# Optimization experiments

Hardware: AMD Instinct MI355X
Metric: run time of the kernel (lower is better)

Reference implementation:

```python
import jax, jax.numpy as jnp
import numpy as np

U, I, D, E = 8192, 8192, 64, 1048576  # users, items, emb dim, nnz of adjacency


def spmm(row, col, val, x, n):
    """Sparse (COO) @ dense: y[r] += val * x[c], like torch.sparse.mm."""
    return jax.ops.segment_sum(val[:, None] * x[col], row, num_segments=n)


def setup_inputs() -> dict:
    key = jax.random.key(0)
    k1, k2, k3, k4, k5, k6 = jax.random.split(key, 6)
    users_emb = jax.random.normal(k1, (U, D), dtype=jnp.float32) * 0.1  # nn.init.normal_(std=0.1)
    items_emb = jax.random.normal(k2, (I, D), dtype=jnp.float32) * 0.1
    edge_row = jax.random.randint(k3, (E,), 0, U + I, dtype=jnp.int32)
    edge_col = jax.random.randint(k4, (E,), 0, U + I, dtype=jnp.int32)
    # positive normalized adjacency values (stand-in for D^-1/2 A D^-1/2 entries)
    edge_val = jax.random.uniform(k5, (E,), dtype=jnp.float32) / 64.0
    # sparse 0/1 interaction matrix densified, as in labels = interaction_mat.toarray()
    labels = (jax.random.uniform(k6, (U, I)) < 0.02).astype(jnp.float32)
    return {"users_emb": users_emb, "items_emb": items_emb,
            "edge_row": edge_row, "edge_col": edge_col,
            "edge_val": edge_val, "labels": labels, "n_layers": 3}


def reference(users_emb, items_emb, edge_row, edge_col, edge_val, labels, n_layers):
    n = users_emb.shape[0] + items_emb.shape[0]
    u = users_emb.shape[0]
    all_emb = jnp.concatenate([users_emb, items_emb], axis=0)  # [n, D]
    # stack + mean over (n_layers+1) layer outputs == online accumulation
    acc = all_emb
    for _ in range(n_layers):
        all_emb = spmm(edge_row, edge_col, edge_val, all_emb, n)
        acc = acc + all_emb
    light_out = acc / jnp.float32(n_layers + 1)
    user_emb = light_out[:u]   # [U, D]
    item_emb = light_out[u:]   # [I, D]
    scores = user_emb @ item_emb.T  # [U, I]
    # BCEWithLogitsLoss (mean reduction): logaddexp(0, s) - s*y
    loss = jnp.mean(jnp.logaddexp(jnp.float32(0.0), scores) - scores * labels)
    return (loss, user_emb, item_emb)
```

## Files before the change

### kernel.cpp

```cpp
#include <hip/hip_runtime.h>

#define U_N 8192
#define N_N 16384
#define E_N 1048576
#define CAP 128
#define CSTRIDE 16

typedef __attribute__((ext_vector_type(8)))  short short8;
typedef __attribute__((ext_vector_type(16))) float f32x16;


__device__ __forceinline__ float bfu(ushort u) {
    union { unsigned v; float f; } c; c.v = (unsigned)u << 16; return c.f;
}
__device__ __forceinline__ ushort f2bf(float f) {
    union { float f; unsigned u; } c; c.f = f;
    return (ushort)((c.u + 0x7fffu + ((c.u >> 16) & 1u)) >> 16);
}

__global__ void k_prep(const float* __restrict__ ue, const float* __restrict__ ie,
                       ushort* __restrict__ xb, float* __restrict__ acc,
                       unsigned* __restrict__ cnt) {
    int i = blockIdx.x * blockDim.x + threadIdx.x;
    const int HU = U_N * 64 / 4;
    float4 v = (i < HU) ? ((const float4*)ue)[i] : ((const float4*)ie)[i - HU];
    ((float4*)acc)[i] = v;
    ushort4 b;
    b.x = f2bf(v.x); b.y = f2bf(v.y); b.z = f2bf(v.z); b.w = f2bf(v.w);
    ((ushort4*)xb)[i] = b;
    if (i < 65536) ((uint4*)cnt)[i] = make_uint4(0, 0, 0, 0);
}

__global__ __launch_bounds__(256) void k_mask(const float* __restrict__ labels,
                                              unsigned* __restrict__ mask) {
    int tid = blockIdx.x * 256 + threadIdx.x;
    const int stride = 2048 * 256;
    #pragma unroll 4
    for (int it = 0; it < 32; ++it) {
        int g = tid + it * stride;
        float4 v = ((const float4*)labels)[g];
        unsigned nib = (v.x != 0.f ? 1u : 0u) | (v.y != 0.f ? 2u : 0u)
                     | (v.z != 0.f ? 4u : 0u) | (v.w != 0.f ? 8u : 0u);
        unsigned wv = nib << ((g & 7) * 4);
        wv |= __shfl_xor(wv, 1);
        wv |= __shfl_xor(wv, 2);
        wv |= __shfl_xor(wv, 4);
        if ((threadIdx.x & 7) == 0) mask[g >> 3] = wv;
    }
}

__global__ void k_bucket(const int* __restrict__ row, const int* __restrict__ col,
                         const float* __restrict__ val, unsigned* __restrict__ cnt,
                         unsigned* __restrict__ buckets) {
    int e = blockIdx.x * blockDim.x + threadIdx.x;
    if (e < E_N) {
        int r = row[e];
        unsigned p = atomicAdd(&cnt[r * CSTRIDE], 1u);
        if (p < CAP)
            buckets[(size_t)r * CAP + p] = (unsigned)col[e] | ((unsigned)f2bf(val[e]) << 16);
    }
}

#define REC_FMA(rec)                                                       \
    {   unsigned _rc = (rec);                                              \
        float _xv = bfu(x[(_rc & 0xFFFFu) * 64 + lane]);                   \
        a = fmaf(bfu((ushort)(_rc >> 16)), _xv, a); }

__global__ void k_spmm(const unsigned* __restrict__ cnt, const unsigned* __restrict__ buckets,
                       const ushort* __restrict__ x, ushort* __restrict__ xo,
                       float* __restrict__ acc) {
    int wave = (int)((blockIdx.x * blockDim.x + threadIdx.x) >> 6);
    int lane = threadIdx.x & 63;
    if (wave >= N_N) return;
    int n = (int)cnt[wave * CSTRIDE]; n = n > CAP ? CAP : n;
    const uint4* bp4 = (const uint4*)(buckets + (size_t)wave * CAP);
    float a = 0.f;
    int j = 0;
    for (; j + 8 <= n; j += 8) {
        uint4 qa = bp4[j >> 2], qb = bp4[(j >> 2) + 1];
        REC_FMA(qa.x) REC_FMA(qa.y) REC_FMA(qa.z) REC_FMA(qa.w)
        REC_FMA(qb.x) REC_FMA(qb.y) REC_FMA(qb.z) REC_FMA(qb.w)
    }
    for (; j < n; ++j) REC_FMA(buckets[(size_t)wave * CAP + j])
    int idx = wave * 64 + lane;
    xo[idx] = f2bf(a);
    acc[idx] += a;
}

__global__ void k_spmm_last(const unsigned* __restrict__ cnt, const unsigned* __restrict__ buckets,
                            const ushort* __restrict__ x, const float* __restrict__ acc,
                            float* __restrict__ o, ushort* __restrict__ bfemb) {
    int wave = (int)((blockIdx.x * blockDim.x + threadIdx.x) >> 6);
    int lane = threadIdx.x & 63;
    if (wave >= N_N) return;
    int n = (int)cnt[wave * CSTRIDE]; n = n > CAP ? CAP : n;
    const uint4* bp4 = (const uint4*)(buckets + (size_t)wave * CAP);
    float a = 0.f;
    int j = 0;
    for (; j + 8 <= n; j += 8) {
        uint4 qa = bp4[j >> 2], qb = bp4[(j >> 2) + 1];
        REC_FMA(qa.x) REC_FMA(qa.y) REC_FMA(qa.z) REC_FMA(qa.w)
        REC_FMA(qb.x) REC_FMA(qb.y) REC_FMA(qb.z) REC_FMA(qb.w)
    }
    for (; j < n; ++j) REC_FMA(buckets[(size_t)wave * CAP + j])
    int idx = wave * 64 + lane;
    float l = (acc[idx] + a) * 0.25f;
    o[idx] = l;
    bfemb[idx] = f2bf(l);
}

__global__ __launch_bounds__(256) void k_gemm_loss(const ushort* __restrict__ bfemb,
                                                   const unsigned* __restrict__ mask,
                                                   float* __restrict__ partials) {
    __shared__ unsigned lmask[128][4];
    __shared__ float red[4];
    int tid  = threadIdx.x;
    int lane = tid & 63;
    int w    = tid >> 6;
    int wr   = w >> 1, wc = w & 1;
    int row0t = blockIdx.y * 128;
    int row0 = row0t + wr * 64;
    int col0 = blockIdx.x * 128 + wc * 64;

    if (tid < 128)
        *(uint4*)&lmask[tid][0] =
            ((const uint4*)mask)[(size_t)(row0t + tid) * 64 + blockIdx.x];

    int lrow = lane & 31;
    int lk   = (lane >> 5) * 8;
    short8 a[2][4], b[2][4];
    #pragma unroll
    for (int fi = 0; fi < 2; ++fi) {
        const ushort* pa = bfemb + (size_t)(row0 + fi * 32 + lrow) * 64 + lk;
        const ushort* pb = bfemb + (size_t)(U_N + col0 + fi * 32 + lrow) * 64 + lk;
        #pragma unroll
        for (int kk = 0; kk < 4; ++kk) {
            a[fi][kk] = *(const short8*)(pa + kk * 16);
            b[fi][kk] = *(const short8*)(pb + kk * 16);
        }
    }

    f32x16 acc00 = {}, acc01 = {}, acc10 = {}, acc11 = {};
    #pragma unroll
    for (int kk = 0; kk < 4; ++kk) {
        acc00 = __builtin_amdgcn_mfma_f32_32x32x16_bf16(a[0][kk], b[0][kk], acc00, 0, 0, 0);
        acc01 = __builtin_amdgcn_mfma_f32_32x32x16_bf16(a[0][kk], b[1][kk], acc01, 0, 0, 0);
        acc10 = __builtin_amdgcn_mfma_f32_32x32x16_bf16(a[1][kk], b[0][kk], acc10, 0, 0, 0);
        acc11 = __builtin_amdgcn_mfma_f32_32x32x16_bf16(a[1][kk], b[1][kk], acc11, 0, 0, 0);
    }

    __syncthreads();

    float sum1 = 0.f, sum2 = 0.f, sum4 = 0.f, sumL = 0.f, m2 = 0.f;
    int rsub = (lane >> 5) * 4;
    int bpos = lane & 31;
    #pragma unroll
    for (int fi = 0; fi < 2; ++fi) {
        #pragma unroll
        for (int q = 0; q < 4; ++q) {
            #pragma unroll
            for (int r = 0; r < 4; ++r) {
                int lr = wr * 64 + fi * 32 + q * 8 + rsub + r;
                unsigned w0 = lmask[lr][wc * 2 + 0];
                unsigned w1 = lmask[lr][wc * 2 + 1];
                #pragma unroll
                for (int fj = 0; fj < 2; ++fj) {
                    const f32x16& ac = fi ? (fj ? acc11 : acc10) : (fj ? acc01 : acc00);
                    float s = ac[q * 4 + r];
                    float labv = (float)(((fj ? w1 : w0) >> bpos) & 1u);
                    float s2 = s * s;
                    sum1 += s;
                    sum2 += s2;
                    sum4 = fmaf(s2, s2, sum4);
                    sumL = fmaf(s, labv, sumL);
                    m2 = fmaxf(m2, s2);
                }
            }
        }
    }

    const float LN2 = 0.69314718055994531f;
    float base = fmaf(0.5f, sum1, fmaf(0.125f, sum2, fmaf(-1.f / 192.f, sum4, 64.f * LN2)));

    if (__any(m2 > 1.0f)) {
        base = 0.f;
        #pragma unroll
        for (int fi = 0; fi < 2; ++fi) {
            #pragma unroll
            for (int fj = 0; fj < 2; ++fj) {
                const f32x16& ac = fi ? (fj ? acc11 : acc10) : (fj ? acc01 : acc00);
                #pragma unroll
                for (int t = 0; t < 16; ++t) {
                    float s = ac[t];
                    base += fmaxf(s, 0.f) + __logf(1.f + __expf(-fabsf(s)));
                }
            }
        }
    }

    float sum = base - sumL;
    #pragma unroll
    for (int off = 32; off > 0; off >>= 1) sum += __shfl_down(sum, off);
    if ((tid & 63) == 0) red[w] = sum;
    __syncthreads();
    if (tid == 0)
        partials[blockIdx.y * 64 + blockIdx.x] = red[0] + red[1] + red[2] + red[3];
}

__global__ __launch_bounds__(256) void k_finish(const float* __restrict__ partials,
                                                float* __restrict__ out) {
    __shared__ float red[4];
    int tid = threadIdx.x;
    float s = 0.f;
    #pragma unroll
    for (int t = 0; t < 4; ++t) {
        float4 v = ((const float4*)partials)[tid + t * 256];
        s += (v.x + v.y) + (v.z + v.w);
    }
    #pragma unroll
    for (int off = 32; off > 0; off >>= 1) s += __shfl_down(s, off);
    if ((tid & 63) == 0) red[tid >> 6] = s;
    __syncthreads();
    if (tid == 0) out[0] = (red[0] + red[1] + red[2] + red[3]) * (1.0f / 67108864.0f);
}

extern "C" void kernel_launch(void* const* d_in, const int* in_sizes, int n_in,
                              void* d_out, int out_size, void* d_ws, size_t ws_size,
                              hipStream_t stream) {
    const float* ue     = (const float*)d_in[0];
    const float* ie     = (const float*)d_in[1];
    const int*   erow   = (const int*)d_in[2];
    const int*   ecol   = (const int*)d_in[3];
    const float* eval_  = (const float*)d_in[4];
    const float* labels = (const float*)d_in[5];
    float* out = (float*)d_out;

    char* ws = (char*)d_ws;
    unsigned* cnt      = (unsigned*)(ws + 0);
    float*    partials = (float*)   (ws + 1048576);
    unsigned* mask     = (unsigned*)(ws + 1064960);
    ushort*   xb0      = (ushort*)  (ws + 9453568);
    ushort*   xb1      = (ushort*)  (ws + 11550720);
    float*    accb     = (float*)   (ws + 13647872);
    ushort*   bfemb    = (ushort*)  (ws + 17842176);
    unsigned* buckets  = (unsigned*)(ws + 19939328);

    k_prep<<<1024, 256, 0, stream>>>(ue, ie, xb0, accb, cnt);
    k_bucket<<<4096, 256, 0, stream>>>(erow, ecol, eval_, cnt, buckets);
    k_mask<<<2048, 256, 0, stream>>>(labels, mask);

    k_spmm<<<4096, 256, 0, stream>>>(cnt, buckets, xb0, xb1, accb);
    k_spmm<<<4096, 256, 0, stream>>>(cnt, buckets, xb1, xb0, accb);
    k_spmm_last<<<4096, 256, 0, stream>>>(cnt, buckets, xb0, accb, out + 1, bfemb);

    dim3 g(64, 64);
    k_gemm_loss<<<g, 256, 0, stream>>>(bfemb, mask, partials);
    k_finish<<<1, 256, 0, stream>>>(partials, out);
}
```

Measured before the change: 245.3 us.

## Enlarge GEMM-loss blocks to 256x128 with swizzled 1D grid and streamed fragment loads

The fused GEMM+BCE kernel now uses 512-thread blocks covering 256 user rows by 128 item columns, launched as a 1D grid of 2048 blocks. Block indices are remapped through an XCD-style swizzle (bid&7) so that neighbouring tiles share L2. A/B fragment loads are moved into the k-loop to cut register pressure under launch_bounds(512,4). The finish kernel reduces half as many partials. This risks lower parallel slack and possible load latency exposure inside the MFMA loop.

Result: slower. 300.4 us (+22.4%).

```diff
diff --git a/kernel.cpp b/kernel.cpp
--- a/kernel.cpp
+++ b/kernel.cpp
@@ -109,44 +109,45 @@
     bfemb[idx] = f2bf(l);
 }
 
-__global__ __launch_bounds__(256) void k_gemm_loss(const ushort* __restrict__ bfemb,
-                                                   const unsigned* __restrict__ mask,
-                                                   float* __restrict__ partials) {
-    __shared__ unsigned lmask[128][4];
-    __shared__ float red[4];
+__global__ __launch_bounds__(512, 4) void k_gemm_loss(const ushort* __restrict__ bfemb,
+                                                      const unsigned* __restrict__ mask,
+                                                      float* __restrict__ partials) {
+    __shared__ unsigned lmask[256][4];
+    __shared__ float red[8];
     int tid  = threadIdx.x;
     int lane = tid & 63;
     int w    = tid >> 6;
     int wr   = w >> 1, wc = w & 1;
-    int row0t = blockIdx.y * 128;
+
+    int bid = blockIdx.x;
+    int idx = (bid & 7) * 256 + (bid >> 3);
+    int by  = idx >> 6;
+    int bx  = idx & 63;
+
+    int row0t = by * 256;
     int row0 = row0t + wr * 64;
-    int col0 = blockIdx.x * 128 + wc * 64;
-
-    if (tid < 128)
+    int col0 = bx * 128 + wc * 64;
+
+    if (tid < 256)
         *(uint4*)&lmask[tid][0] =
-            ((const uint4*)mask)[(size_t)(row0t + tid) * 64 + blockIdx.x];
+            ((const uint4*)mask)[(size_t)(row0t + tid) * 64 + bx];
 
     int lrow = lane & 31;
     int lk   = (lane >> 5) * 8;
-    short8 a[2][4], b[2][4];
-    #pragma unroll
-    for (int fi = 0; fi < 2; ++fi) {
-        const ushort* pa = bfemb + (size_t)(row0 + fi * 32 + lrow) * 64 + lk;
-        const ushort* pb = bfemb + (size_t)(U_N + col0 + fi * 32 + lrow) * 64 + lk;
-        #pragma unroll
-        for (int kk = 0; kk < 4; ++kk) {
-            a[fi][kk] = *(const short8*)(pa + kk * 16);
-            b[fi][kk] = *(const short8*)(pb + kk * 16);
-        }
-    }
+    const ushort* pa0 = bfemb + (size_t)(row0 + lrow) * 64 + lk;
+    const ushort* pb0 = bfemb + (size_t)(U_N + col0 + lrow) * 64 + lk;
 
     f32x16 acc00 = {}, acc01 = {}, acc10 = {}, acc11 = {};
     #pragma unroll
     for (int kk = 0; kk < 4; ++kk) {
-        acc00 = __builtin_amdgcn_mfma_f32_32x32x16_bf16(a[0][kk], b[0][kk], acc00, 0, 0, 0);
-        acc01 = __builtin_amdgcn_mfma_f32_32x32x16_bf16(a[0][kk], b[1][kk], acc01, 0, 0, 0);
-        acc10 = __builtin_amdgcn_mfma_f32_32x32x16_bf16(a[1][kk], b[0][kk], acc10, 0, 0, 0);
-        acc11 = __builtin_amdgcn_mfma_f32_32x32x16_bf16(a[1][kk], b[1][kk], acc11, 0, 0, 0);
+        short8 a0 = *(const short8*)(pa0 + kk * 16);
+        short8 a1 = *(const short8*)(pa0 + 32 * 64 + kk * 16);
+        short8 b0 = *(const short8*)(pb0 + kk * 16);
+        short8 b1 = *(const short8*)(pb0 + 32 * 64 + kk * 16);
+        acc00 = __builtin_amdgcn_mfma_f32_32x32x16_bf16(a0, b0, acc00, 0, 0, 0);
+        acc01 = __builtin_amdgcn_mfma_f32_32x32x16_bf16(a0, b1, acc01, 0, 0, 0);
+        acc10 = __builtin_amdgcn_mfma_f32_32x32x16_bf16(a1, b0, acc10, 0, 0, 0);
+        acc11 = __builtin_amdgcn_mfma_f32_32x32x16_bf16(a1, b1, acc11, 0, 0, 0);
     }
 
     __syncthreads();
@@ -203,8 +204,12 @@
     for (int off = 32; off > 0; off >>= 1) sum += __shfl_down(sum, off);
     if ((tid & 63) == 0) red[w] = sum;
     __syncthreads();
-    if (tid == 0)
-        partials[blockIdx.y * 64 + blockIdx.x] = red[0] + red[1] + red[2] + red[3];
+    if (tid == 0) {
+        float t = 0.f;
+        #pragma unroll
+        for (int i = 0; i < 8; ++i) t += red[i];
+        partials[bid] = t;
+    }
 }
 
 __global__ __launch_bounds__(256) void k_finish(const float* __restrict__ partials,
@@ -213,7 +218,7 @@
     int tid = threadIdx.x;
     float s = 0.f;
     #pragma unroll
-    for (int t = 0; t < 4; ++t) {
+    for (int t = 0; t < 2; ++t) {
         float4 v = ((const float4*)partials)[tid + t * 256];
         s += (v.x + v.y) + (v.z + v.w);
     }
@@ -253,7 +258,6 @@
     k_spmm<<<4096, 256, 0, stream>>>(cnt, buckets, xb1, xb0, accb);
     k_spmm_last<<<4096, 256, 0, stream>>>(cnt, buckets, xb0, accb, out + 1, bfemb);
 
-    dim3 g(64, 64);
-    k_gemm_loss<<<g, 256, 0, stream>>>(bfemb, mask, partials);
+    k_gemm_loss<<<2048, 512, 0, stream>>>(bfemb, mask, partials);
     k_finish<<<1, 256, 0, stream>>>(partials, out);
 }
```
